# Kernel tuning notes

Measured on AMD Instinct MI355X. Metric: run time of the kernel, lower is better.

Reference implementation:

```python
import jax, jax.numpy as jnp
import numpy as np

B, C, F = 4, 3, 51
H_OUT, W_OUT = 384, 384
H_IN, W_IN = H_OUT + F - 1, W_OUT + F - 1


def setup_inputs() -> dict:
    key = jax.random.key(0)
    k1, k2, k3 = jax.random.split(key, 3)
    tenIn = jax.random.normal(k1, (B, C, H_IN, W_IN), dtype=jnp.float32)
    tenVer = jax.random.uniform(k2, (B, F, H_OUT, W_OUT), dtype=jnp.float32)
    tenHor = jax.random.uniform(k3, (B, F, H_OUT, W_OUT), dtype=jnp.float32)
    return {"tenIn": tenIn, "tenVer": tenVer, "tenHor": tenHor}


def reference(tenIn, tenVer, tenHor):
    # Out[n,c,y,x] = sum_{fy,fx} In[n,c,y+fy,x+fx] * Ver[n,fy,y,x] * Hor[n,fx,y,x]
    b, c, h_in, w_in = tenIn.shape
    f = tenVer.shape[1]
    h_out, w_out = tenVer.shape[2], tenVer.shape[3]

    # Horizontal sliding windows of the input, built once (static slices):
    # wx[b,c,fx,y_in,x] = In[b,c,y_in,x+fx]  -> [B,C,F,H_in,W_out]
    wx = jnp.stack([tenIn[:, :, :, fx:fx + w_out] for fx in range(f)], axis=2)

    def step(acc, fy):
        # rows[b,c,fx,y,x] = In[b,c,y+fy,x+fx]  -> [B,C,F,H_out,W_out]
        rows = jax.lax.dynamic_slice_in_dim(wx, fy, h_out, axis=3)
        # horizontal contraction with per-pixel horizontal kernel
        a = jnp.einsum('bcfyx,bfyx->bcyx', rows, tenHor)
        # weight by per-pixel vertical kernel tap fy
        ver_fy = jax.lax.dynamic_slice_in_dim(tenVer, fy, 1, axis=1)  # [B,1,H,W]
        return acc + a * ver_fy, None

    out0 = jnp.zeros((b, c, h_out, w_out), dtype=tenIn.dtype)
    out, _ = jax.lax.scan(step, out0, jnp.arange(f))
    return out
```

## Files before the change

### kernel.cpp

```cpp
#include <hip/hip_runtime.h>

namespace {
constexpr int CC = 3, FF = 51;
constexpr int BB = 4;
constexpr int HOUT = 384, WOUT = 384;
constexpr int HIN = 434, WIN = 434;
constexpr int KY = 4;
constexpr int LANES = 64;
constexpr int NW = 4;
constexpr int EXT = LANES + FF - 1;
constexpr int LPAD = 128;
constexpr int NSTEP = FF + KY - 1;
constexpr int NSG = CC * LPAD / LANES;
constexpr int NQW = 4;
constexpr int NPW = 8;
constexpr int SSTRIDE = NW * CC * LPAD;
constexpr size_t IN16_BYTES = (size_t)BB * CC * HIN * WIN * 2;

using half2v = _Float16 __attribute__((ext_vector_type(2)));

__device__ __forceinline__ float fdot2f(half2v a, half2v b, float c) {
#if __has_builtin(__builtin_amdgcn_fdot2)
  return __builtin_amdgcn_fdot2(a, b, c, false);
#else
  return c + (float)a.x * (float)b.x + (float)a.y * (float)b.y;
#endif
}

#define GLLDS(G, L)                                                  \
  __builtin_amdgcn_global_load_lds(                                  \
      (const __attribute__((address_space(1))) void*)(G),            \
      (__attribute__((address_space(3))) void*)(L), 4, 0, 0)
}

__global__ void cvt16_kernel(const float* __restrict__ in,
                             unsigned int* __restrict__ out, int n2) {
  int i = blockIdx.x * blockDim.x + threadIdx.x;
  const int stride = gridDim.x * blockDim.x;
  for (; i < n2; i += stride) {
    const float2 v = *reinterpret_cast<const float2*>(in + 2 * (size_t)i);
    const unsigned short lo = __builtin_bit_cast(unsigned short, (_Float16)v.x);
    const unsigned short hi = __builtin_bit_cast(unsigned short, (_Float16)v.y);
    out[i] = ((unsigned int)hi << 16) | lo;
  }
}

template <bool DMA>
__global__ __launch_bounds__(NW* LANES, 2) void sepconv_kernel(
    const float* __restrict__ In, const float* __restrict__ Ver,
    const float* __restrict__ Hor, float* __restrict__ Out,
    const unsigned short* __restrict__ In16) {
  const int lane = threadIdx.x;
  const int w = threadIdx.y;
  const int x0 = blockIdx.x * LANES;
  const int y0 = blockIdx.y * KY;
  const int b = blockIdx.z;
  const int x = x0 + lane;
  const int fxBase = 13 * w;
  const int ntaps = (w < 3) ? 13 : 12;
  const int aw = (lane + fxBase) & 3;
  const int bw = lane + fxBase - aw;

  __shared__ __align__(16) unsigned short sIn[2][NW][CC][LPAD];
  __shared__ float sRed[NW - 1][CC][KY][LANES];
  unsigned short* const sflat = &sIn[0][0][0][0];

  const size_t HW = (size_t)HOUT * WOUT;

  half2v hp[KY][NPW];
  {
    const float* horx = Hor + (size_t)b * FF * HW + x;
#pragma unroll
    for (int t = 0; t < KY; ++t) {
      const float* hb = horx + (size_t)(y0 + t) * WOUT;
#pragma unroll
      for (int j = 0; j < NPW; ++j) {
        const int u0 = 2 * j - aw;
        const int u1 = u0 + 1;
        float f0 = (u0 >= 0 && u0 < ntaps) ? hb[(size_t)(fxBase + u0) * HW] : 0.0f;
        float f1 = (u1 >= 0 && u1 < ntaps) ? hb[(size_t)(fxBase + u1) * HW] : 0.0f;
        half2v p;
        p.x = (_Float16)f0;
        p.y = (_Float16)f1;
        hp[t][j] = p;
      }
    }
  }

  const float* inb = In + ((size_t)b * CC * HIN + y0) * WIN + x0;
  const float* verb = Ver + (size_t)b * FF * HW + (size_t)y0 * WOUT + x;
  const unsigned short* in16b =
      In16 + ((size_t)b * CC * HIN + y0) * WIN + x0;
  const int vmax = 2 * WIN - 4 - 2 * x0;
  const int voff = (4 * lane < vmax) ? 4 * lane : vmax;

  float acc[CC][KY] = {};
  float sv[NSG];

#define STAGE_LOAD(R)                                                         \
  _Pragma("unroll") for (int k = 0; k < NSG; ++k) {                           \
    const int e = lane + (k & 1) * 64;                                        \
    const bool valid = ((k & 1) == 0) || (lane < EXT - LANES);                \
    sv[k] = valid ? inb[(size_t)((k >> 1) * HIN + (R)) * WIN + e] : 0.0f;     \
  }

#define STAGE_WRITE(BF)                                                       \
  _Pragma("unroll") for (int k = 0; k < NSG; ++k) {                           \
    const int e = lane + (k & 1) * 64;                                        \
    sflat[(BF)*SSTRIDE + (w * CC + (k >> 1)) * LPAD + e] =                    \
        __builtin_bit_cast(unsigned short, (_Float16)sv[k]);                  \
  }

#define STAGE_DMA(R, BF)                                                      \
  _Pragma("unroll") for (int c = 0; c < CC; ++c) {                            \
    const unsigned short* g = in16b + (size_t)(c * HIN + (R)) * WIN;          \
    GLLDS((const char*)g + voff, &sIn[BF][w][c][0]);                          \
  }

#define COMPUTE(R, BF)                                                        \
  {                                                                           \
    float vv[KY];                                                             \
    _Pragma("unroll") for (int t = 0; t < KY; ++t) {                          \
      const int u = (R)-t;                                                    \
      vv[t] = (u >= 0 && u < FF)                                              \
                  ? verb[(size_t)u * HW + (size_t)t * WOUT]                   \
                  : 0.0f;                                                     \
    }                                                                         \
    _Pragma("unroll") for (int c = 0; c < CC; ++c) {                          \
      const unsigned short* rp = sflat + (BF)*SSTRIDE + (w * CC + c) * LPAD + bw; \
      float d[KY] = {};                                                       \
      _Pragma("unroll") for (int q = 0; q < NQW; ++q) {                       \
        const uint2 u2 = *reinterpret_cast<const uint2*>(rp + 4 * q);         \
        const half2v p0 = __builtin_bit_cast(half2v, u2.x);                   \
        const half2v p1 = __builtin_bit_cast(half2v, u2.y);                   \
        _Pragma("unroll") for (int t = 0; t < KY; ++t) {                      \
          d[t] = fdot2f(p0, hp[t][2 * q], d[t]);                              \
          d[t] = fdot2f(p1, hp[t][2 * q + 1], d[t]);                          \
        }                                                                     \
      }                                                                       \
      _Pragma("unroll") for (int t = 0; t < KY; ++t) acc[c][t] += d[t] * vv[t];\
    }                                                                         \
  }

  if constexpr (DMA) {
    STAGE_DMA(0, 0);
#pragma unroll 2
    for (int r = 0; r < NSTEP; ++r) {
      const int rn = (r + 1 < NSTEP) ? r + 1 : NSTEP - 1;
      STAGE_DMA(rn, (r + 1) & 1);
      COMPUTE(r, r & 1);
    }
  } else {
    STAGE_LOAD(0);
    STAGE_WRITE(0);
#pragma unroll 1
    for (int r = 0; r < NSTEP; r += 2) {
      STAGE_LOAD(r + 1);
      COMPUTE(r, 0);
      STAGE_WRITE(1);
      const bool more = (r + 2 < NSTEP);
      if (more) { STAGE_LOAD(r + 2); }
      COMPUTE(r + 1, 1);
      if (more) { STAGE_WRITE(0); }
    }
  }

  if (w > 0) {
#pragma unroll
    for (int c = 0; c < CC; ++c)
#pragma unroll
      for (int t = 0; t < KY; ++t) sRed[w - 1][c][t][lane] = acc[c][t];
  }
  __syncthreads();
  if (w == 0) {
    float* outb = Out + (size_t)b * CC * HW + (size_t)y0 * WOUT + x0 + lane;
#pragma unroll
    for (int c = 0; c < CC; ++c)
#pragma unroll
      for (int t = 0; t < KY; ++t)
        outb[(size_t)c * HW + (size_t)t * WOUT] =
            acc[c][t] + sRed[0][c][t][lane] + sRed[1][c][t][lane] +
            sRed[2][c][t][lane];
  }
#undef STAGE_LOAD
#undef STAGE_WRITE
#undef STAGE_DMA
#undef COMPUTE
}

extern "C" void kernel_launch(void* const* d_in, const int* in_sizes, int n_in,
                              void* d_out, int out_size, void* d_ws, size_t ws_size,
                              hipStream_t stream) {
  const float* In = (const float*)d_in[0];
  const float* Ver = (const float*)d_in[1];
  const float* Hor = (const float*)d_in[2];
  float* Out = (float*)d_out;

  dim3 grid(WOUT / LANES, HOUT / KY, BB);
  dim3 block(LANES, NW, 1);

  if (ws_size >= IN16_BYTES && d_ws != nullptr) {
    const int n2 = (int)(BB * CC * HIN * WIN / 2);
    cvt16_kernel<<<2048, 256, 0, stream>>>(In, (unsigned int*)d_ws, n2);
    sepconv_kernel<true><<<grid, block, 0, stream>>>(
        In, Ver, Hor, Out, (const unsigned short*)d_ws);
  } else {
    sepconv_kernel<false><<<grid, block, 0, stream>>>(In, Ver, Hor, Out,
                                                      nullptr);
  }
}
```

Baseline: 162.2 us.

## Peel DMA row loop and add explicit LDS waitcnt fences between stages

Restructures the DMA pipeline loop: the first three and last three rows are peeled off, so the steady-state loop loads the vertical weights without bounds checks. It inserts an explicit s_waitcnt lgkmcnt(0) plus a scheduling barrier before each new global-to-LDS DMA issue, so the row buffer is known to be ready before the next prefetch overwrites the other one. It also seeds the dot accumulators from the first dot2 instead of zero and uses fma for the vertical weighting. The intent is to cut predicate and select overhead in the hot loop and to make the double-buffer ordering explicit. The fences and scheduling barriers may serialise memory latency the compiler could otherwise overlap.

```diff
diff --git a/kernel.cpp b/kernel.cpp
--- a/kernel.cpp
+++ b/kernel.cpp
@@ -31,6 +31,10 @@
   __builtin_amdgcn_global_load_lds(                                  \
       (const __attribute__((address_space(1))) void*)(G),            \
       (__attribute__((address_space(3))) void*)(L), 4, 0, 0)
+
+#define LDS_FENCE()                                                  \
+  asm volatile("s_waitcnt lgkmcnt(0)" ::: "memory");                 \
+  __builtin_amdgcn_sched_barrier(0)
 }
 
 __global__ void cvt16_kernel(const float* __restrict__ in,
@@ -89,6 +93,11 @@
 
   const float* inb = In + ((size_t)b * CC * HIN + y0) * WIN + x0;
   const float* verb = Ver + (size_t)b * FF * HW + (size_t)y0 * WOUT + x;
+  const float* vbase0 = Ver + (size_t)b * FF * HW + (size_t)(y0 + 0) * WOUT + x0;
+  const float* vbase1 = Ver + (size_t)b * FF * HW + (size_t)(y0 + 1) * WOUT + x0;
+  const float* vbase2 = Ver + (size_t)b * FF * HW + (size_t)(y0 + 2) * WOUT + x0;
+  const float* vbase3 = Ver + (size_t)b * FF * HW + (size_t)(y0 + 3) * WOUT + x0;
+
   const unsigned short* in16b =
       In16 + ((size_t)b * CC * HIN + y0) * WIN + x0;
   const int vmax = 2 * WIN - 4 - 2 * x0;
@@ -117,7 +126,33 @@
     GLLDS((const char*)g + voff, &sIn[BF][w][c][0]);                          \
   }
 
-#define COMPUTE(R, BF)                                                        \
+#define DOT_CORE(BF)                                                          \
+    _Pragma("unroll") for (int c = 0; c < CC; ++c) {                          \
+      const unsigned short* rp = sflat + (BF)*SSTRIDE + (w * CC + c) * LPAD + bw; \
+      float d[KY];                                                            \
+      {                                                                       \
+        const uint2 u2 = *reinterpret_cast<const uint2*>(rp);                 \
+        const half2v p0 = __builtin_bit_cast(half2v, u2.x);                   \
+        const half2v p1 = __builtin_bit_cast(half2v, u2.y);                   \
+        _Pragma("unroll") for (int t = 0; t < KY; ++t) {                      \
+          d[t] = fdot2f(p0, hp[t][0], 0.0f);                                  \
+          d[t] = fdot2f(p1, hp[t][1], d[t]);                                  \
+        }                                                                     \
+      }                                                                       \
+      _Pragma("unroll") for (int q = 1; q < NQW; ++q) {                       \
+        const uint2 u2 = *reinterpret_cast<const uint2*>(rp + 4 * q);         \
+        const half2v p0 = __builtin_bit_cast(half2v, u2.x);                   \
+        const half2v p1 = __builtin_bit_cast(half2v, u2.y);                   \
+        _Pragma("unroll") for (int t = 0; t < KY; ++t) {                      \
+          d[t] = fdot2f(p0, hp[t][2 * q], d[t]);                              \
+          d[t] = fdot2f(p1, hp[t][2 * q + 1], d[t]);                          \
+        }                                                                     \
+      }                                                                       \
+      _Pragma("unroll") for (int t = 0; t < KY; ++t)                          \
+        acc[c][t] = __builtin_fmaf(d[t], vv[t], acc[c][t]);                   \
+    }
+
+#define COMPUTE_G(R, BF)                                                      \
   {                                                                           \
     float vv[KY];                                                             \
     _Pragma("unroll") for (int t = 0; t < KY; ++t) {                          \
@@ -126,41 +161,56 @@
                   ? verb[(size_t)u * HW + (size_t)t * WOUT]                   \
                   : 0.0f;                                                     \
     }                                                                         \
-    _Pragma("unroll") for (int c = 0; c < CC; ++c) {                          \
-      const unsigned short* rp = sflat + (BF)*SSTRIDE + (w * CC + c) * LPAD + bw; \
-      float d[KY] = {};                                                       \
-      _Pragma("unroll") for (int q = 0; q < NQW; ++q) {                       \
-        const uint2 u2 = *reinterpret_cast<const uint2*>(rp + 4 * q);         \
-        const half2v p0 = __builtin_bit_cast(half2v, u2.x);                   \
-        const half2v p1 = __builtin_bit_cast(half2v, u2.y);                   \
-        _Pragma("unroll") for (int t = 0; t < KY; ++t) {                      \
-          d[t] = fdot2f(p0, hp[t][2 * q], d[t]);                              \
-          d[t] = fdot2f(p1, hp[t][2 * q + 1], d[t]);                          \
-        }                                                                     \
-      }                                                                       \
-      _Pragma("unroll") for (int t = 0; t < KY; ++t) acc[c][t] += d[t] * vv[t];\
-    }                                                                         \
+    DOT_CORE(BF)                                                              \
+  }
+
+#define COMPUTE_S(R, BF)                                                      \
+  {                                                                           \
+    float vv[KY];                                                             \
+    vv[0] = vbase0[(size_t)((R)-0) * HW + lane];                              \
+    vv[1] = vbase1[(size_t)((R)-1) * HW + lane];                              \
+    vv[2] = vbase2[(size_t)((R)-2) * HW + lane];                              \
+    vv[3] = vbase3[(size_t)((R)-3) * HW + lane];                              \
+    DOT_CORE(BF)                                                              \
   }
 
   if constexpr (DMA) {
     STAGE_DMA(0, 0);
-#pragma unroll 2
-    for (int r = 0; r < NSTEP; ++r) {
-      const int rn = (r + 1 < NSTEP) ? r + 1 : NSTEP - 1;
-      STAGE_DMA(rn, (r + 1) & 1);
-      COMPUTE(r, r & 1);
-    }
+    STAGE_DMA(1, 1);
+    COMPUTE_G(0, 0);
+    LDS_FENCE();
+    STAGE_DMA(2, 0);
+    COMPUTE_G(1, 1);
+    LDS_FENCE();
+    STAGE_DMA(3, 1);
+    COMPUTE_G(2, 0);
+#pragma unroll 1
+    for (int r = 3; r < FF; r += 2) {
+      LDS_FENCE();
+      STAGE_DMA(r + 1, 0);
+      COMPUTE_S(r, 1);
+      LDS_FENCE();
+      STAGE_DMA(r + 2, 1);
+      COMPUTE_S(r + 1, 0);
+    }
+    LDS_FENCE();
+    STAGE_DMA(52, 0);
+    COMPUTE_G(51, 1);
+    LDS_FENCE();
+    STAGE_DMA(53, 1);
+    COMPUTE_G(52, 0);
+    COMPUTE_G(53, 1);
   } else {
     STAGE_LOAD(0);
     STAGE_WRITE(0);
 #pragma unroll 1
     for (int r = 0; r < NSTEP; r += 2) {
       STAGE_LOAD(r + 1);
-      COMPUTE(r, 0);
+      COMPUTE_G(r, 0);
       STAGE_WRITE(1);
       const bool more = (r + 2 < NSTEP);
       if (more) { STAGE_LOAD(r + 2); }
-      COMPUTE(r + 1, 1);
+      COMPUTE_G(r + 1, 1);
       if (more) { STAGE_WRITE(0); }
     }
   }
@@ -185,7 +235,9 @@
 #undef STAGE_LOAD
 #undef STAGE_WRITE
 #undef STAGE_DMA
-#undef COMPUTE
+#undef DOT_CORE
+#undef COMPUTE_G
+#undef COMPUTE_S
 }
 
 extern "C" void kernel_launch(void* const* d_in, const int* in_sizes, int n_in,
```

New measurement: 160.5 us. Within noise of the previous version (-1.0%).

## Triple-buffer LDS DMA pipeline and prefetch vertical weights one step ahead

Applied to the files above, without the earlier changes.

Extends the per-wave LDS staging from two to three buffers, so input rows are DMA'd two steps ahead of use. The Ver taps for the next row are loaded into rotating register sets before the current row's compute, with unguarded loads in the steady state. The main loop is unrolled by three, with peeled prologue and epilogue steps. Explicit lgkmcnt waits with scheduling barriers replace the implicit ordering. The aim is to hide global and DMA latency behind the dot-product work, at the cost of more LDS, more registers and a fragile hand-written wait scheme.

```diff
diff --git a/kernel.cpp b/kernel.cpp
--- a/kernel.cpp
+++ b/kernel.cpp
@@ -31,6 +31,10 @@
   __builtin_amdgcn_global_load_lds(                                  \
       (const __attribute__((address_space(1))) void*)(G),            \
       (__attribute__((address_space(3))) void*)(L), 4, 0, 0)
+
+#define LDS_FENCE()                                                  \
+  asm volatile("s_waitcnt lgkmcnt(0)" ::: "memory");                 \
+  __builtin_amdgcn_sched_barrier(0)
 }
 
 __global__ void cvt16_kernel(const float* __restrict__ in,
@@ -61,7 +65,7 @@
   const int aw = (lane + fxBase) & 3;
   const int bw = lane + fxBase - aw;
 
-  __shared__ __align__(16) unsigned short sIn[2][NW][CC][LPAD];
+  __shared__ __align__(16) unsigned short sIn[3][NW][CC][LPAD];
   __shared__ float sRed[NW - 1][CC][KY][LANES];
   unsigned short* const sflat = &sIn[0][0][0][0];
 
@@ -89,6 +93,11 @@
 
   const float* inb = In + ((size_t)b * CC * HIN + y0) * WIN + x0;
   const float* verb = Ver + (size_t)b * FF * HW + (size_t)y0 * WOUT + x;
+  const float* vbase0 = Ver + (size_t)b * FF * HW + (size_t)(y0 + 0) * WOUT + x0;
+  const float* vbase1 = Ver + (size_t)b * FF * HW + (size_t)(y0 + 1) * WOUT + x0;
+  const float* vbase2 = Ver + (size_t)b * FF * HW + (size_t)(y0 + 2) * WOUT + x0;
+  const float* vbase3 = Ver + (size_t)b * FF * HW + (size_t)(y0 + 3) * WOUT + x0;
+
   const unsigned short* in16b =
       In16 + ((size_t)b * CC * HIN + y0) * WIN + x0;
   const int vmax = 2 * WIN - 4 - 2 * x0;
@@ -96,6 +105,7 @@
 
   float acc[CC][KY] = {};
   float sv[NSG];
+  float vvA[KY], vvB[KY], vvC[KY];
 
 #define STAGE_LOAD(R)                                                         \
   _Pragma("unroll") for (int k = 0; k < NSG; ++k) {                           \
@@ -117,19 +127,35 @@
     GLLDS((const char*)g + voff, &sIn[BF][w][c][0]);                          \
   }
 
-#define COMPUTE(R, BF)                                                        \
+#define VV_S(R, V)                                                            \
+  V[0] = vbase0[(size_t)((R)-0) * HW + lane];                                 \
+  V[1] = vbase1[(size_t)((R)-1) * HW + lane];                                 \
+  V[2] = vbase2[(size_t)((R)-2) * HW + lane];                                 \
+  V[3] = vbase3[(size_t)((R)-3) * HW + lane];
+
+#define VV_G(R, V)                                                            \
+  _Pragma("unroll") for (int t = 0; t < KY; ++t) {                            \
+    const int u = (R)-t;                                                      \
+    V[t] = (u >= 0 && u < FF)                                                 \
+               ? verb[(size_t)u * HW + (size_t)t * WOUT]                      \
+               : 0.0f;                                                        \
+  }
+
+#define COMPUTE(BF, V)                                                        \
   {                                                                           \
-    float vv[KY];                                                             \
-    _Pragma("unroll") for (int t = 0; t < KY; ++t) {                          \
-      const int u = (R)-t;                                                    \
-      vv[t] = (u >= 0 && u < FF)                                              \
-                  ? verb[(size_t)u * HW + (size_t)t * WOUT]                   \
-                  : 0.0f;                                                     \
-    }                                                                         \
     _Pragma("unroll") for (int c = 0; c < CC; ++c) {                          \
       const unsigned short* rp = sflat + (BF)*SSTRIDE + (w * CC + c) * LPAD + bw; \
-      float d[KY] = {};                                                       \
-      _Pragma("unroll") for (int q = 0; q < NQW; ++q) {                       \
+      float d[KY];                                                            \
+      {                                                                       \
+        const uint2 u2 = *reinterpret_cast<const uint2*>(rp);                 \
+        const half2v p0 = __builtin_bit_cast(half2v, u2.x);                   \
+        const half2v p1 = __builtin_bit_cast(half2v, u2.y);                   \
+        _Pragma("unroll") for (int t = 0; t < KY; ++t) {                      \
+          d[t] = fdot2f(p0, hp[t][0], 0.0f);                                  \
+          d[t] = fdot2f(p1, hp[t][1], d[t]);                                  \
+        }                                                                     \
+      }                                                                       \
+      _Pragma("unroll") for (int q = 1; q < NQW; ++q) {                       \
         const uint2 u2 = *reinterpret_cast<const uint2*>(rp + 4 * q);         \
         const half2v p0 = __builtin_bit_cast(half2v, u2.x);                   \
         const half2v p1 = __builtin_bit_cast(half2v, u2.y);                   \
@@ -138,29 +164,43 @@
           d[t] = fdot2f(p1, hp[t][2 * q + 1], d[t]);                          \
         }                                                                     \
       }                                                                       \
-      _Pragma("unroll") for (int t = 0; t < KY; ++t) acc[c][t] += d[t] * vv[t];\
+      _Pragma("unroll") for (int t = 0; t < KY; ++t)                          \
+        acc[c][t] = __builtin_fmaf(d[t], V[t], acc[c][t]);                    \
     }                                                                         \
   }
 
   if constexpr (DMA) {
     STAGE_DMA(0, 0);
-#pragma unroll 2
-    for (int r = 0; r < NSTEP; ++r) {
-      const int rn = (r + 1 < NSTEP) ? r + 1 : NSTEP - 1;
-      STAGE_DMA(rn, (r + 1) & 1);
-      COMPUTE(r, r & 1);
+    STAGE_DMA(1, 1);
+    VV_G(0, vvA);
+    LDS_FENCE(); STAGE_DMA(2, 2); VV_G(1, vvB); COMPUTE(0, vvA);
+    LDS_FENCE(); STAGE_DMA(3, 0); VV_G(2, vvC); COMPUTE(1, vvB);
+    LDS_FENCE(); STAGE_DMA(4, 1); VV_S(3, vvA); COMPUTE(2, vvC);
+#pragma unroll 1
+    for (int r = 3; r < 48; r += 3) {
+      LDS_FENCE(); STAGE_DMA(r + 2, 2); VV_S(r + 1, vvB); COMPUTE(0, vvA);
+      LDS_FENCE(); STAGE_DMA(r + 3, 0); VV_S(r + 2, vvC); COMPUTE(1, vvB);
+      LDS_FENCE(); STAGE_DMA(r + 4, 1); VV_S(r + 3, vvA); COMPUTE(2, vvC);
     }
+    LDS_FENCE(); STAGE_DMA(50, 2); VV_S(49, vvB); COMPUTE(0, vvA);
+    LDS_FENCE(); STAGE_DMA(51, 0); VV_S(50, vvC); COMPUTE(1, vvB);
+    LDS_FENCE(); STAGE_DMA(52, 1); VV_G(51, vvA); COMPUTE(2, vvC);
+    LDS_FENCE(); STAGE_DMA(53, 2); VV_G(52, vvB); COMPUTE(0, vvA);
+    LDS_FENCE(); VV_G(53, vvC); COMPUTE(1, vvB);
+    COMPUTE(2, vvC);
   } else {
     STAGE_LOAD(0);
     STAGE_WRITE(0);
 #pragma unroll 1
     for (int r = 0; r < NSTEP; r += 2) {
       STAGE_LOAD(r + 1);
-      COMPUTE(r, 0);
+      VV_G(r, vvA);
+      COMPUTE(0, vvA);
       STAGE_WRITE(1);
       const bool more = (r + 2 < NSTEP);
       if (more) { STAGE_LOAD(r + 2); }
-      COMPUTE(r + 1, 1);
+      VV_G(r + 1, vvB);
+      COMPUTE(1, vvB);
       if (more) { STAGE_WRITE(0); }
     }
   }
@@ -185,6 +225,8 @@
 #undef STAGE_LOAD
 #undef STAGE_WRITE
 #undef STAGE_DMA
+#undef VV_S
+#undef VV_G
 #undef COMPUTE
 }
 
```

New measurement: 179.8 us. 1.11x slower.
